# Performance work log

Measured on AMD Instinct MI355X. Metric: run time of the kernel, lower is better.

## Reference

```python
import jax, jax.numpy as jnp
import numpy as np

B, S, H, D = 8, 16, 32, 64
HID = H * D
PAST = 4096


def setup_inputs() -> dict:
    key = jax.random.key(0)
    ks = jax.random.split(key, 7)
    sc = 0.02
    return {
        "hidden_states": jax.random.normal(ks[0], (B, S, HID), jnp.float32),
        "past_k": jax.random.normal(ks[1], (B, H, PAST, D), jnp.float32),
        "past_v": jax.random.normal(ks[2], (B, H, PAST, D), jnp.float32),
        "wq": jax.random.normal(ks[3], (HID, HID), jnp.float32) * sc,
        "wk": jax.random.normal(ks[4], (HID, HID), jnp.float32) * sc,
        "wv": jax.random.normal(ks[5], (HID, HID), jnp.float32) * sc,
        "wo": jax.random.normal(ks[6], (HID, HID), jnp.float32) * sc,
    }


def reference(hidden_states, past_k, past_v, wq, wk, wv, wo):
    b, s, _ = hidden_states.shape
    # QKV projections (torch Linear: x @ W.T), split into heads -> [B,H,S,D]
    q = (hidden_states @ wq.T).reshape(b, s, H, D).transpose(0, 2, 1, 3)
    k = (hidden_states @ wk.T).reshape(b, s, H, D).transpose(0, 2, 1, 3)
    v = (hidden_states @ wv.T).reshape(b, s, H, D).transpose(0, 2, 1, 3)
    # KV-cache concat: [B,H,past+S,D]
    k = jnp.concatenate([past_k, k], axis=2)
    v = jnp.concatenate([past_v, v], axis=2)
    scale = 1.0 / jnp.sqrt(jnp.asarray(D, hidden_states.dtype))
    # scores [B,H,S,T]
    scores = jnp.einsum("bhsd,bhtd->bhst", q, k) * scale
    probs = jax.nn.softmax(scores, axis=-1)
    out = jnp.einsum("bhst,bhtd->bhsd", probs, v)
    out = out.transpose(0, 2, 1, 3).reshape(b, s, HID)
    return out @ wo.T
```

## Files before the change

### kernel.cpp

```cpp
#include <hip/hip_runtime.h>
#include <hip/hip_bf16.h>
#include <stdint.h>

#define HID 2048
#define NH  32
#define HD  64
#define NB  8
#define NS  16
#define PAST 4096

#define QSCALE 0.18033688011112042591f

typedef __attribute__((ext_vector_type(8))) short short8;
typedef __attribute__((ext_vector_type(4))) short short4v;
typedef __attribute__((ext_vector_type(4))) float f32x4;

#define MFMA(a, b, c) __builtin_amdgcn_mfma_f32_16x16x32_bf16((a), (b), (c), 0, 0, 0)

#define PART_STRIDE 1088
#define NSPLIT 4
#define NTILES 16

static __device__ __forceinline__ short f2bf(float f) {
    __hip_bfloat16 h = __float2bfloat16(f);
    return *reinterpret_cast<short*>(&h);
}

static __device__ __forceinline__ void gload_lds16(const float* g, float* l) {
    __builtin_amdgcn_global_load_lds(
        (const __attribute__((address_space(1))) void*)(g),
        (__attribute__((address_space(3))) void*)(l),
        16, 0, 0);
}

static __device__ __forceinline__ short8 pack8(float4 a, float4 b) {
    short8 r;
    r[0] = f2bf(a.x); r[1] = f2bf(a.y); r[2] = f2bf(a.z); r[3] = f2bf(a.w);
    r[4] = f2bf(b.x); r[5] = f2bf(b.y); r[6] = f2bf(b.z); r[7] = f2bf(b.w);
    return r;
}

static __device__ __forceinline__ short8 pack8s(float4 a, float4 b, float s) {
    short8 r;
    r[0] = f2bf(a.x * s); r[1] = f2bf(a.y * s); r[2] = f2bf(a.z * s); r[3] = f2bf(a.w * s);
    r[4] = f2bf(b.x * s); r[5] = f2bf(b.y * s); r[6] = f2bf(b.z * s); r[7] = f2bf(b.w * s);
    return r;
}

__global__ __launch_bounds__(256) void cvt_kernel(const float* __restrict__ in,
                                                  short* __restrict__ out) {
    int i = (blockIdx.x * 256 + threadIdx.x) * 4;
    float4 v = *reinterpret_cast<const float4*>(in + i);
    short4v o;
    o[0] = f2bf(v.x); o[1] = f2bf(v.y); o[2] = f2bf(v.z); o[3] = f2bf(v.w);
    *reinterpret_cast<short4v*>(out + i) = o;
}

__global__ __launch_bounds__(128) void proj_kernel(
        const short* __restrict__ X,
        const float* __restrict__ W0, const float* __restrict__ W1,
        const float* __restrict__ W2,
        float* __restrict__ Y0, float* __restrict__ Y1, float* __restrict__ Y2) {
    int mat   = blockIdx.x >> 9;
    int rest  = blockIdx.x & 511;
    int strip = rest >> 2, ks = rest & 3;
    int nbase = strip * 16;
    int k0    = ks * 512;
    const float* W = (mat == 0) ? W0 : (mat == 1) ? W1 : W2;
    float*       Y = (mat == 0) ? Y0 : (mat == 1) ? Y1 : Y2;

    int lane = threadIdx.x & 63;
    int wave = threadIdx.x >> 6;
    int lr = lane & 15, g = lane >> 4;

    f32x4 acc0 = {0.f, 0.f, 0.f, 0.f};
    f32x4 acc1 = {0.f, 0.f, 0.f, 0.f};
    f32x4 acc2 = {0.f, 0.f, 0.f, 0.f};
    f32x4 acc3 = {0.f, 0.f, 0.f, 0.f};

    const short* xr = X + (size_t)(wave * 64 + lr) * HID + g * 8 + k0;
    const float* wr = W + (size_t)(nbase + lr) * HID + g * 8 + k0;

    #pragma unroll 4
    for (int kc = 0; kc < 512; kc += 32) {
        float4 w0 = *reinterpret_cast<const float4*>(wr + kc);
        float4 w1 = *reinterpret_cast<const float4*>(wr + kc + 4);
        short8 bb = pack8(w0, w1);
        short8 a0 = *reinterpret_cast<const short8*>(xr + kc);
        short8 a1 = *reinterpret_cast<const short8*>(xr + (size_t)16 * HID + kc);
        short8 a2 = *reinterpret_cast<const short8*>(xr + (size_t)32 * HID + kc);
        short8 a3 = *reinterpret_cast<const short8*>(xr + (size_t)48 * HID + kc);
        acc0 = MFMA(a0, bb, acc0);
        acc1 = MFMA(a1, bb, acc1);
        acc2 = MFMA(a2, bb, acc2);
        acc3 = MFMA(a3, bb, acc3);
    }
    #define STACC(accv, f) do { \
        atomicAdd(&Y[(size_t)(wave * 64 + (f) * 16 + (g << 2) + 0) * HID + nbase + lr], accv[0]); \
        atomicAdd(&Y[(size_t)(wave * 64 + (f) * 16 + (g << 2) + 1) * HID + nbase + lr], accv[1]); \
        atomicAdd(&Y[(size_t)(wave * 64 + (f) * 16 + (g << 2) + 2) * HID + nbase + lr], accv[2]); \
        atomicAdd(&Y[(size_t)(wave * 64 + (f) * 16 + (g << 2) + 3) * HID + nbase + lr], accv[3]); \
    } while (0)
    STACC(acc0, 0); STACC(acc1, 1); STACC(acc2, 2); STACC(acc3, 3);
    #undef STACC
}

__global__ __launch_bounds__(256, 4) void attn_kernel(
        const float* __restrict__ q,
        const float* __restrict__ knew, const float* __restrict__ vnew,
        const float* __restrict__ pastK, const float* __restrict__ pastV,
        float* __restrict__ parts) {
    __shared__ __align__(16) float lds_v[2][64 * 64];
    __shared__ float s_m[4][16];
    __shared__ float s_l[4][16];

    int bid = blockIdx.x;
    int bh = bid >> 2, split = bid & 3;
    int b = bh >> 5, h = bh & 31;
    int wave = threadIdx.x >> 6, lane = threadIdx.x & 63;
    int lq = lane & 15, g = lane >> 4;

    const float* qp = q + (size_t)(b * NS + lq) * HID + h * HD + g * 8;
    short8 qf0, qf1;
    {
        float4 a0 = *reinterpret_cast<const float4*>(qp);
        float4 a1 = *reinterpret_cast<const float4*>(qp + 4);
        float4 a2 = *reinterpret_cast<const float4*>(qp + 32);
        float4 a3 = *reinterpret_cast<const float4*>(qp + 36);
        qf0 = pack8s(a0, a1, QSCALE);
        qf1 = pack8s(a2, a3, QSCALE);
    }

    f32x4 o0 = {0.f, 0.f, 0.f, 0.f};
    f32x4 o1 = {0.f, 0.f, 0.f, 0.f};
    f32x4 o2 = {0.f, 0.f, 0.f, 0.f};
    f32x4 o3 = {0.f, 0.f, 0.f, 0.f};
    float m = -__builtin_inff(), lsum = 0.0f;

    const float* ksplit = pastK + (size_t)bh * PAST * HD + (size_t)split * 1024 * HD;
    const float* vsplit = pastV + (size_t)bh * PAST * HD + (size_t)split * 1024 * HD;

    #define STAGE(tt, dstf) do { \
        const float* gsrc_ = vsplit + (size_t)(tt) * 64 * HD; \
        gload_lds16(gsrc_ + (wave * 4 + 0) * 256 + lane * 4, (dstf) + (wave * 4 + 0) * 256); \
        gload_lds16(gsrc_ + (wave * 4 + 1) * 256 + lane * 4, (dstf) + (wave * 4 + 1) * 256); \
        gload_lds16(gsrc_ + (wave * 4 + 2) * 256 + lane * 4, (dstf) + (wave * 4 + 2) * 256); \
        gload_lds16(gsrc_ + (wave * 4 + 3) * 256 + lane * 4, (dstf) + (wave * 4 + 3) * 256); \
    } while (0)

    STAGE(0, lds_v[0]);
    __syncthreads();

    int cur = 0;
    #pragma unroll 1
    for (int t = 0; t < NTILES; ++t) {
        if (t + 1 < NTILES) STAGE(t + 1, lds_v[cur ^ 1]);

        const float* kr = ksplit + (size_t)(t * 64 + wave * 16 + lq) * HD + (g << 3);
        float4 ka = *reinterpret_cast<const float4*>(kr);
        float4 kb = *reinterpret_cast<const float4*>(kr + 4);
        float4 kc = *reinterpret_cast<const float4*>(kr + 32);
        float4 kd = *reinterpret_cast<const float4*>(kr + 36);
        short8 af0 = pack8(ka, kb);
        short8 af1 = pack8(kc, kd);
        f32x4 sv = {0.f, 0.f, 0.f, 0.f};
        sv = MFMA(af0, qf0, sv);
        sv = MFMA(af1, qf1, sv);

        float tmax = fmaxf(fmaxf(sv[0], sv[1]), fmaxf(sv[2], sv[3]));
        tmax = fmaxf(tmax, __shfl_xor(tmax, 16));
        tmax = fmaxf(tmax, __shfl_xor(tmax, 32));
        float mn = fmaxf(m, tmax);
        float alpha = exp2f(m - mn);
        float e0 = exp2f(sv[0] - mn);
        float e1 = exp2f(sv[1] - mn);
        float e2 = exp2f(sv[2] - mn);
        float e3 = exp2f(sv[3] - mn);
        float rsum = e0 + e1 + e2 + e3;
        rsum += __shfl_xor(rsum, 16);
        rsum += __shfl_xor(rsum, 32);
        lsum = lsum * alpha + rsum;
        m = mn;
        o0 *= alpha; o1 *= alpha; o2 *= alpha; o3 *= alpha;

        short8 pf;
        pf[0] = f2bf(e0); pf[1] = f2bf(e1); pf[2] = f2bf(e2); pf[3] = f2bf(e3);
        pf[4] = 0; pf[5] = 0; pf[6] = 0; pf[7] = 0;

        const float* vc = lds_v[cur] + (wave * 16 + (g << 2)) * 64;
        #define VFR(dst, dcol) do { \
            dst[0] = f2bf(vc[0 * 64 + (dcol)]); \
            dst[1] = f2bf(vc[1 * 64 + (dcol)]); \
            dst[2] = f2bf(vc[2 * 64 + (dcol)]); \
            dst[3] = f2bf(vc[3 * 64 + (dcol)]); \
            dst[4] = 0; dst[5] = 0; dst[6] = 0; dst[7] = 0; \
        } while (0)
        {
            short8 vf;
            VFR(vf, lq);       o0 = MFMA(vf, pf, o0);
            VFR(vf, 16 + lq);  o1 = MFMA(vf, pf, o1);
            VFR(vf, 32 + lq);  o2 = MFMA(vf, pf, o2);
            VFR(vf, 48 + lq);  o3 = MFMA(vf, pf, o3);
        }
        #undef VFR

        __syncthreads();
        cur ^= 1;
    }
    #undef STAGE

    if (split == 0 && wave == 0) {
        const float* kr = knew + (size_t)(b * NS + lq) * HID + h * HD + g * 8;
        float4 ka = *reinterpret_cast<const float4*>(kr);
        float4 kb2 = *reinterpret_cast<const float4*>(kr + 4);
        float4 kc2 = *reinterpret_cast<const float4*>(kr + 32);
        float4 kd2 = *reinterpret_cast<const float4*>(kr + 36);
        short8 af0 = pack8(ka, kb2);
        short8 af1 = pack8(kc2, kd2);
        f32x4 sv = {0.f, 0.f, 0.f, 0.f};
        sv = MFMA(af0, qf0, sv);
        sv = MFMA(af1, qf1, sv);

        float tmax = fmaxf(fmaxf(sv[0], sv[1]), fmaxf(sv[2], sv[3]));
        tmax = fmaxf(tmax, __shfl_xor(tmax, 16));
        tmax = fmaxf(tmax, __shfl_xor(tmax, 32));
        float mn = fmaxf(m, tmax);
        float alpha = exp2f(m - mn);
        float e0 = exp2f(sv[0] - mn);
        float e1 = exp2f(sv[1] - mn);
        float e2 = exp2f(sv[2] - mn);
        float e3 = exp2f(sv[3] - mn);
        float rsum = e0 + e1 + e2 + e3;
        rsum += __shfl_xor(rsum, 16);
        rsum += __shfl_xor(rsum, 32);
        lsum = lsum * alpha + rsum;
        m = mn;
        o0 *= alpha; o1 *= alpha; o2 *= alpha; o3 *= alpha;

        short8 pfT;
        pfT[0] = f2bf(e0); pfT[1] = f2bf(e1); pfT[2] = f2bf(e2); pfT[3] = f2bf(e3);
        pfT[4] = 0; pfT[5] = 0; pfT[6] = 0; pfT[7] = 0;

        const float* vt2 = vnew + (size_t)(b * NS) * HID + h * HD;
        #define LOADVT(dst, dcol) do { \
            dst[0] = f2bf(vt2[(size_t)((g << 2) + 0) * HID + (dcol)]); \
            dst[1] = f2bf(vt2[(size_t)((g << 2) + 1) * HID + (dcol)]); \
            dst[2] = f2bf(vt2[(size_t)((g << 2) + 2) * HID + (dcol)]); \
            dst[3] = f2bf(vt2[(size_t)((g << 2) + 3) * HID + (dcol)]); \
            dst[4] = 0; dst[5] = 0; dst[6] = 0; dst[7] = 0; \
        } while (0)
        short8 vv0, vv1, vv2, vv3;
        LOADVT(vv0, lq); LOADVT(vv1, 16 + lq); LOADVT(vv2, 32 + lq); LOADVT(vv3, 48 + lq);
        #undef LOADVT
        o0 = MFMA(vv0, pfT, o0);
        o1 = MFMA(vv1, pfT, o1);
        o2 = MFMA(vv2, pfT, o2);
        o3 = MFMA(vv3, pfT, o3);
    }

    float* so_w = (float*)lds_v[0] + wave * 1024;
    #define STO(ov, dt) do { \
        so_w[lq * 64 + (dt) * 16 + (g << 2) + 0] = ov[0]; \
        so_w[lq * 64 + (dt) * 16 + (g << 2) + 1] = ov[1]; \
        so_w[lq * 64 + (dt) * 16 + (g << 2) + 2] = ov[2]; \
        so_w[lq * 64 + (dt) * 16 + (g << 2) + 3] = ov[3]; \
    } while (0)
    STO(o0, 0); STO(o1, 1); STO(o2, 2); STO(o3, 3);
    #undef STO
    if (g == 0) { s_m[wave][lq] = m; s_l[wave][lq] = lsum; }
    __syncthreads();

    if (wave == 0) {
        float M = fmaxf(fmaxf(s_m[0][lq], s_m[1][lq]), fmaxf(s_m[2][lq], s_m[3][lq]));
        float aw0 = exp2f(s_m[0][lq] - M);
        float aw1 = exp2f(s_m[1][lq] - M);
        float aw2 = exp2f(s_m[2][lq] - M);
        float aw3 = exp2f(s_m[3][lq] - M);
        float L = aw0 * s_l[0][lq] + aw1 * s_l[1][lq] + aw2 * s_l[2][lq] + aw3 * s_l[3][lq];
        const float* so0 = (const float*)lds_v[0] + 0 * 1024;
        const float* so1 = (const float*)lds_v[0] + 1 * 1024;
        const float* so2 = (const float*)lds_v[0] + 2 * 1024;
        const float* so3 = (const float*)lds_v[0] + 3 * 1024;
        float* pbase = parts + (size_t)bid * PART_STRIDE;
        if (g == 0) { pbase[lq] = M; pbase[16 + lq] = L; }
        for (int dd = 0; dd < 16; ++dd) {
            int di = g * 16 + dd;
            float v = aw0 * so0[lq * 64 + di] + aw1 * so1[lq * 64 + di] +
                      aw2 * so2[lq * 64 + di] + aw3 * so3[lq * 64 + di];
            pbase[32 + lq * 64 + di] = v;
        }
    }
}

__global__ __launch_bounds__(256) void merge_kernel(const float* __restrict__ parts,
                                                    short* __restrict__ attnb) {
    int bh = blockIdx.x;
    int tid = threadIdx.x;
    int qi = tid >> 4, ds = (tid & 15) * 4;
    const float* p0 = parts + (size_t)(bh * NSPLIT) * PART_STRIDE;
    const float* p1 = p0 + PART_STRIDE;
    const float* p2 = p1 + PART_STRIDE;
    const float* p3 = p2 + PART_STRIDE;
    float m0 = p0[qi], m1 = p1[qi], m2 = p2[qi], m3 = p3[qi];
    float M = fmaxf(fmaxf(m0, m1), fmaxf(m2, m3));
    float a0 = exp2f(m0 - M), a1 = exp2f(m1 - M), a2 = exp2f(m2 - M), a3 = exp2f(m3 - M);
    float inv = 1.0f / (a0 * p0[16 + qi] + a1 * p1[16 + qi] +
                        a2 * p2[16 + qi] + a3 * p3[16 + qi]);
    int b = bh >> 5, h = bh & 31;
    int base = 32 + qi * 64 + ds;
    float v0 = (a0 * p0[base + 0] + a1 * p1[base + 0] + a2 * p2[base + 0] + a3 * p3[base + 0]) * inv;
    float v1 = (a0 * p0[base + 1] + a1 * p1[base + 1] + a2 * p2[base + 1] + a3 * p3[base + 1]) * inv;
    float v2 = (a0 * p0[base + 2] + a1 * p1[base + 2] + a2 * p2[base + 2] + a3 * p3[base + 2]) * inv;
    float v3 = (a0 * p0[base + 3] + a1 * p1[base + 3] + a2 * p2[base + 3] + a3 * p3[base + 3]) * inv;
    short4v o;
    o[0] = f2bf(v0); o[1] = f2bf(v1); o[2] = f2bf(v2); o[3] = f2bf(v3);
    *reinterpret_cast<short4v*>(attnb + (size_t)(b * NS + qi) * HID + h * HD + ds) = o;
}

extern "C" void kernel_launch(void* const* d_in, const int* in_sizes, int n_in,
                              void* d_out, int out_size, void* d_ws, size_t ws_size,
                              hipStream_t stream) {
    const float* hs     = (const float*)d_in[0];
    const float* past_k = (const float*)d_in[1];
    const float* past_v = (const float*)d_in[2];
    const float* wq     = (const float*)d_in[3];
    const float* wk     = (const float*)d_in[4];
    const float* wv     = (const float*)d_in[5];
    const float* wo     = (const float*)d_in[6];
    float* out = (float*)d_out;

    float* qb = (float*)d_ws;
    float* kn = qb + 128 * 2048;
    float* vn = kn + 128 * 2048;
    short* hsb   = (short*)(vn + 128 * 2048);
    short* attnb = hsb + 128 * 2048;
    float* parts = (float*)(attnb + 128 * 2048);

    hipMemsetAsync(qb, 0, (size_t)3 * 128 * 2048 * sizeof(float), stream);
    hipMemsetAsync(out, 0, (size_t)128 * 2048 * sizeof(float), stream);

    cvt_kernel<<<256, 256, 0, stream>>>(hs, hsb);
    proj_kernel<<<1536, 128, 0, stream>>>(hsb, wq, wk, wv, qb, kn, vn);
    attn_kernel<<<256 * NSPLIT, 256, 0, stream>>>(qb, kn, vn, past_k, past_v, parts);
    merge_kernel<<<256, 256, 0, stream>>>(parts, attnb);
    proj_kernel<<<512, 128, 0, stream>>>(attnb, wo, wo, wo, out, out, out);
}
```

Measured before the change: 170.3 us.

## Replace atomic split-K with partial buffers and prefetch K tiles without block barriers

The projection kernel no longer accumulates its split-K results with atomicAdd into zeroed outputs. Each K split now writes its own partial buffer, and a new merge4 kernel sums the four partials; this removes the two memsets and the atomic contention. The attention loop is unrolled by two with register double-buffering of K loads and per-wave V staging into LDS, and the per-tile __syncthreads is dropped. That is safe only because each wave reads only the V rows it staged itself. The cost is extra partial-buffer traffic, an extra launch, and a reliance on the compiler placing the waits for the async LDS loads correctly.

Result: no change. 169.0 us (-0.7%).

```diff
diff --git a/kernel.cpp b/kernel.cpp
--- a/kernel.cpp
+++ b/kernel.cpp
@@ -19,7 +19,7 @@
 
 #define PART_STRIDE 1088
 #define NSPLIT 4
-#define NTILES 16
+#define MATSZ (128 * HID)
 
 static __device__ __forceinline__ short f2bf(float f) {
     __hip_bfloat16 h = __float2bfloat16(f);
@@ -60,14 +60,14 @@
         const short* __restrict__ X,
         const float* __restrict__ W0, const float* __restrict__ W1,
         const float* __restrict__ W2,
-        float* __restrict__ Y0, float* __restrict__ Y1, float* __restrict__ Y2) {
+        float* __restrict__ Yp) {
     int mat   = blockIdx.x >> 9;
     int rest  = blockIdx.x & 511;
     int strip = rest >> 2, ks = rest & 3;
     int nbase = strip * 16;
     int k0    = ks * 512;
     const float* W = (mat == 0) ? W0 : (mat == 1) ? W1 : W2;
-    float*       Y = (mat == 0) ? Y0 : (mat == 1) ? Y1 : Y2;
+    float* Y = Yp + (size_t)(mat * 4 + ks) * MATSZ;
 
     int lane = threadIdx.x & 63;
     int wave = threadIdx.x >> 6;
@@ -96,13 +96,33 @@
         acc3 = MFMA(a3, bb, acc3);
     }
     #define STACC(accv, f) do { \
-        atomicAdd(&Y[(size_t)(wave * 64 + (f) * 16 + (g << 2) + 0) * HID + nbase + lr], accv[0]); \
-        atomicAdd(&Y[(size_t)(wave * 64 + (f) * 16 + (g << 2) + 1) * HID + nbase + lr], accv[1]); \
-        atomicAdd(&Y[(size_t)(wave * 64 + (f) * 16 + (g << 2) + 2) * HID + nbase + lr], accv[2]); \
-        atomicAdd(&Y[(size_t)(wave * 64 + (f) * 16 + (g << 2) + 3) * HID + nbase + lr], accv[3]); \
+        Y[(size_t)(wave * 64 + (f) * 16 + (g << 2) + 0) * HID + nbase + lr] = accv[0]; \
+        Y[(size_t)(wave * 64 + (f) * 16 + (g << 2) + 1) * HID + nbase + lr] = accv[1]; \
+        Y[(size_t)(wave * 64 + (f) * 16 + (g << 2) + 2) * HID + nbase + lr] = accv[2]; \
+        Y[(size_t)(wave * 64 + (f) * 16 + (g << 2) + 3) * HID + nbase + lr] = accv[3]; \
     } while (0)
     STACC(acc0, 0); STACC(acc1, 1); STACC(acc2, 2); STACC(acc3, 3);
     #undef STACC
+}
+
+__global__ __launch_bounds__(256) void merge4_kernel(
+        const float* __restrict__ Yp,
+        float* __restrict__ Y0, float* __restrict__ Y1, float* __restrict__ Y2) {
+    int mat = blockIdx.x >> 8;
+    int blk = blockIdx.x & 255;
+    float* Y = (mat == 0) ? Y0 : (mat == 1) ? Y1 : Y2;
+    const float* P = Yp + (size_t)mat * 4 * MATSZ;
+    int idx = blk * 1024 + threadIdx.x * 4;
+    float4 a = *reinterpret_cast<const float4*>(P + idx);
+    float4 b = *reinterpret_cast<const float4*>(P + MATSZ + idx);
+    float4 c = *reinterpret_cast<const float4*>(P + 2 * MATSZ + idx);
+    float4 d = *reinterpret_cast<const float4*>(P + 3 * MATSZ + idx);
+    float4 s;
+    s.x = a.x + b.x + c.x + d.x;
+    s.y = a.y + b.y + c.y + d.y;
+    s.z = a.z + b.z + c.z + d.z;
+    s.w = a.w + b.w + c.w + d.w;
+    *reinterpret_cast<float4*>(Y + idx) = s;
 }
 
 __global__ __launch_bounds__(256, 4) void attn_kernel(
@@ -140,74 +160,81 @@
     const float* ksplit = pastK + (size_t)bh * PAST * HD + (size_t)split * 1024 * HD;
     const float* vsplit = pastV + (size_t)bh * PAST * HD + (size_t)split * 1024 * HD;
 
-    #define STAGE(tt, dstf) do { \
-        const float* gsrc_ = vsplit + (size_t)(tt) * 64 * HD; \
+    #define ISSUE_K(T, A, Bv, C, D) do { \
+        const float* kr_ = ksplit + (size_t)((T) * 64 + wave * 16 + lq) * HD + (g << 3); \
+        A  = *reinterpret_cast<const float4*>(kr_); \
+        Bv = *reinterpret_cast<const float4*>(kr_ + 4); \
+        C  = *reinterpret_cast<const float4*>(kr_ + 32); \
+        D  = *reinterpret_cast<const float4*>(kr_ + 36); \
+    } while (0)
+
+    #define STAGE(T, dstf) do { \
+        const float* gsrc_ = vsplit + (size_t)(T) * 64 * HD; \
         gload_lds16(gsrc_ + (wave * 4 + 0) * 256 + lane * 4, (dstf) + (wave * 4 + 0) * 256); \
         gload_lds16(gsrc_ + (wave * 4 + 1) * 256 + lane * 4, (dstf) + (wave * 4 + 1) * 256); \
         gload_lds16(gsrc_ + (wave * 4 + 2) * 256 + lane * 4, (dstf) + (wave * 4 + 2) * 256); \
         gload_lds16(gsrc_ + (wave * 4 + 3) * 256 + lane * 4, (dstf) + (wave * 4 + 3) * 256); \
     } while (0)
 
+    #define COMPUTE(A, Bv, C, D, BUF) do { \
+        short8 af0 = pack8(A, Bv); \
+        short8 af1 = pack8(C, D); \
+        f32x4 sv = {0.f, 0.f, 0.f, 0.f}; \
+        sv = MFMA(af0, qf0, sv); \
+        sv = MFMA(af1, qf1, sv); \
+        float tmax = fmaxf(fmaxf(sv[0], sv[1]), fmaxf(sv[2], sv[3])); \
+        tmax = fmaxf(tmax, __shfl_xor(tmax, 16)); \
+        tmax = fmaxf(tmax, __shfl_xor(tmax, 32)); \
+        float mn = fmaxf(m, tmax); \
+        float alpha = exp2f(m - mn); \
+        float e0 = exp2f(sv[0] - mn); \
+        float e1 = exp2f(sv[1] - mn); \
+        float e2 = exp2f(sv[2] - mn); \
+        float e3 = exp2f(sv[3] - mn); \
+        float rsum = e0 + e1 + e2 + e3; \
+        rsum += __shfl_xor(rsum, 16); \
+        rsum += __shfl_xor(rsum, 32); \
+        lsum = lsum * alpha + rsum; \
+        m = mn; \
+        o0 *= alpha; o1 *= alpha; o2 *= alpha; o3 *= alpha; \
+        short8 pf; \
+        pf[0] = f2bf(e0); pf[1] = f2bf(e1); pf[2] = f2bf(e2); pf[3] = f2bf(e3); \
+        pf[4] = 0; pf[5] = 0; pf[6] = 0; pf[7] = 0; \
+        const float* vc = lds_v[BUF] + (wave * 16 + (g << 2)) * 64; \
+        short8 vf; \
+        vf[0] = f2bf(vc[0 * 64 + lq]);      vf[1] = f2bf(vc[1 * 64 + lq]); \
+        vf[2] = f2bf(vc[2 * 64 + lq]);      vf[3] = f2bf(vc[3 * 64 + lq]); \
+        vf[4] = 0; vf[5] = 0; vf[6] = 0; vf[7] = 0; \
+        o0 = MFMA(vf, pf, o0); \
+        vf[0] = f2bf(vc[0 * 64 + 16 + lq]); vf[1] = f2bf(vc[1 * 64 + 16 + lq]); \
+        vf[2] = f2bf(vc[2 * 64 + 16 + lq]); vf[3] = f2bf(vc[3 * 64 + 16 + lq]); \
+        o1 = MFMA(vf, pf, o1); \
+        vf[0] = f2bf(vc[0 * 64 + 32 + lq]); vf[1] = f2bf(vc[1 * 64 + 32 + lq]); \
+        vf[2] = f2bf(vc[2 * 64 + 32 + lq]); vf[3] = f2bf(vc[3 * 64 + 32 + lq]); \
+        o2 = MFMA(vf, pf, o2); \
+        vf[0] = f2bf(vc[0 * 64 + 48 + lq]); vf[1] = f2bf(vc[1 * 64 + 48 + lq]); \
+        vf[2] = f2bf(vc[2 * 64 + 48 + lq]); vf[3] = f2bf(vc[3 * 64 + 48 + lq]); \
+        o3 = MFMA(vf, pf, o3); \
+    } while (0)
+
+    float4 kA0, kA1, kA2, kA3, kB0, kB1, kB2, kB3;
+    ISSUE_K(0, kA0, kA1, kA2, kA3);
     STAGE(0, lds_v[0]);
-    __syncthreads();
-
-    int cur = 0;
+
     #pragma unroll 1
-    for (int t = 0; t < NTILES; ++t) {
-        if (t + 1 < NTILES) STAGE(t + 1, lds_v[cur ^ 1]);
-
-        const float* kr = ksplit + (size_t)(t * 64 + wave * 16 + lq) * HD + (g << 3);
-        float4 ka = *reinterpret_cast<const float4*>(kr);
-        float4 kb = *reinterpret_cast<const float4*>(kr + 4);
-        float4 kc = *reinterpret_cast<const float4*>(kr + 32);
-        float4 kd = *reinterpret_cast<const float4*>(kr + 36);
-        short8 af0 = pack8(ka, kb);
-        short8 af1 = pack8(kc, kd);
-        f32x4 sv = {0.f, 0.f, 0.f, 0.f};
-        sv = MFMA(af0, qf0, sv);
-        sv = MFMA(af1, qf1, sv);
-
-        float tmax = fmaxf(fmaxf(sv[0], sv[1]), fmaxf(sv[2], sv[3]));
-        tmax = fmaxf(tmax, __shfl_xor(tmax, 16));
-        tmax = fmaxf(tmax, __shfl_xor(tmax, 32));
-        float mn = fmaxf(m, tmax);
-        float alpha = exp2f(m - mn);
-        float e0 = exp2f(sv[0] - mn);
-        float e1 = exp2f(sv[1] - mn);
-        float e2 = exp2f(sv[2] - mn);
-        float e3 = exp2f(sv[3] - mn);
-        float rsum = e0 + e1 + e2 + e3;
-        rsum += __shfl_xor(rsum, 16);
-        rsum += __shfl_xor(rsum, 32);
-        lsum = lsum * alpha + rsum;
-        m = mn;
-        o0 *= alpha; o1 *= alpha; o2 *= alpha; o3 *= alpha;
-
-        short8 pf;
-        pf[0] = f2bf(e0); pf[1] = f2bf(e1); pf[2] = f2bf(e2); pf[3] = f2bf(e3);
-        pf[4] = 0; pf[5] = 0; pf[6] = 0; pf[7] = 0;
-
-        const float* vc = lds_v[cur] + (wave * 16 + (g << 2)) * 64;
-        #define VFR(dst, dcol) do { \
-            dst[0] = f2bf(vc[0 * 64 + (dcol)]); \
-            dst[1] = f2bf(vc[1 * 64 + (dcol)]); \
-            dst[2] = f2bf(vc[2 * 64 + (dcol)]); \
-            dst[3] = f2bf(vc[3 * 64 + (dcol)]); \
-            dst[4] = 0; dst[5] = 0; dst[6] = 0; dst[7] = 0; \
-        } while (0)
-        {
-            short8 vf;
-            VFR(vf, lq);       o0 = MFMA(vf, pf, o0);
-            VFR(vf, 16 + lq);  o1 = MFMA(vf, pf, o1);
-            VFR(vf, 32 + lq);  o2 = MFMA(vf, pf, o2);
-            VFR(vf, 48 + lq);  o3 = MFMA(vf, pf, o3);
+    for (int tt = 0; tt < 8; ++tt) {
+        ISSUE_K(2 * tt + 1, kB0, kB1, kB2, kB3);
+        STAGE(2 * tt + 1, lds_v[1]);
+        COMPUTE(kA0, kA1, kA2, kA3, 0);
+        if (tt < 7) {
+            ISSUE_K(2 * tt + 2, kA0, kA1, kA2, kA3);
+            STAGE(2 * tt + 2, lds_v[0]);
         }
-        #undef VFR
-
-        __syncthreads();
-        cur ^= 1;
-    }
+        COMPUTE(kB0, kB1, kB2, kB3, 1);
+    }
+    #undef COMPUTE
     #undef STAGE
+    #undef ISSUE_K
 
     if (split == 0 && wave == 0) {
         const float* kr = knew + (size_t)(b * NS + lq) * HID + h * HD + g * 8;
@@ -329,19 +356,20 @@
     const float* wo     = (const float*)d_in[6];
     float* out = (float*)d_out;
 
-    float* qb = (float*)d_ws;
-    float* kn = qb + 128 * 2048;
-    float* vn = kn + 128 * 2048;
-    short* hsb   = (short*)(vn + 128 * 2048);
-    short* attnb = hsb + 128 * 2048;
-    float* parts = (float*)(attnb + 128 * 2048);
-
-    hipMemsetAsync(qb, 0, (size_t)3 * 128 * 2048 * sizeof(float), stream);
-    hipMemsetAsync(out, 0, (size_t)128 * 2048 * sizeof(float), stream);
+    float* qb    = (float*)d_ws;
+    float* kn    = qb + MATSZ;
+    float* vn    = kn + MATSZ;
+    short* hsb   = (short*)(vn + MATSZ);
+    short* attnb = hsb + MATSZ;
+    float* parts = (float*)(attnb + MATSZ);
+    float* qkvp  = parts + 1024 * PART_STRIDE;
+    float* op    = qkvp + 3 * 4 * MATSZ;
 
     cvt_kernel<<<256, 256, 0, stream>>>(hs, hsb);
-    proj_kernel<<<1536, 128, 0, stream>>>(hsb, wq, wk, wv, qb, kn, vn);
+    proj_kernel<<<1536, 128, 0, stream>>>(hsb, wq, wk, wv, qkvp);
+    merge4_kernel<<<768, 256, 0, stream>>>(qkvp, qb, kn, vn);
     attn_kernel<<<256 * NSPLIT, 256, 0, stream>>>(qb, kn, vn, past_k, past_v, parts);
     merge_kernel<<<256, 256, 0, stream>>>(parts, attnb);
-    proj_kernel<<<512, 128, 0, stream>>>(attnb, wo, wo, wo, out, out, out);
-}
+    proj_kernel<<<512, 128, 0, stream>>>(attnb, wo, wo, wo, op);
+    merge4_kernel<<<256, 256, 0, stream>>>(op, out, out, out);
+}
```
